# Kernel optimization log

Measured on AMD Instinct MI355X. Metric: run time of the kernel, lower is better.

The kernel has to match this reference:

```python
import jax, jax.numpy as jnp
import numpy as np
from jax import lax

WINDOW_SIZE = 11
EPS = 1e-6  # params.epsilon (external global in original repo)
FACTOR = 255.0  # 2**8 - 1
C1 = 0.01
C2 = 10.0
# Constants from TMQI paper (computed with numpy, static)
_CSF = 100.0 * 2.6 * (0.0192 + 0.114 * 16) * np.exp(-(0.114 * 16) ** 1.1)
U_HDR = 128.0 / (1.4 * _CSF)
SIG_HDR = U_HDR / 3.0
U_LDR = U_HDR
SIG_LDR = U_LDR / 3.0


def _norm_cdf(x, loc, scale):
    return 0.5 * (1.0 + lax.erf((x - loc) / (scale * np.sqrt(2.0).astype(np.float32))))


def _box_conv(x, w):
    # x: [B,1,H,W], w: [1,1,ws,ws] (uniform window summing to 1), VALID padding
    return lax.conv_general_dilated(
        x, w, window_strides=(1, 1), padding='VALID',
        dimension_numbers=('NCHW', 'OIHW', 'NCHW'))


def setup_inputs() -> dict:
    key = jax.random.key(0)
    k1, k2 = jax.random.split(key)
    img1 = jax.random.uniform(k1, (16, 1, 1024, 1024), dtype=jnp.float32)
    img2 = jax.random.uniform(k2, (16, 1, 1024, 1024), dtype=jnp.float32)
    return {"img1": img1, "img2": img2}


def reference(img1, img2):
    # create_window returns ones((1, channel, ws, ws)); normalized -> uniform 1/ws^2
    ws = WINDOW_SIZE
    window = jnp.ones((1, 1, ws, ws), dtype=img1.dtype) / (ws * ws)

    # Global min/max normalization to [0, 255]
    x1 = FACTOR * (img1 - img1.min()) / (img1.max() - img1.min() + EPS)
    x2 = FACTOR * (img2 - img2.min()) / (img2.max() - img2.min() + EPS)

    mu1 = _box_conv(x1, window)
    mu2 = _box_conv(x2, window)
    mu1_sq = mu1 * mu1
    mu2_sq = mu2 * mu2
    mu1_mu2 = mu1 * mu2

    sigma1_sq = _box_conv(x1 * x1, window) - mu1_sq
    sigma2_sq = _box_conv(x2 * x2, window) - mu2_sq
    sigma12 = _box_conv(x1 * x2, window) - mu1_mu2

    sigma1 = jnp.sqrt(jnp.maximum(sigma1_sq, 0.0) + EPS)
    sigma2 = jnp.sqrt(jnp.maximum(sigma2_sq, 0.0) + EPS)

    sigma1p = _norm_cdf(sigma1, U_HDR, SIG_HDR)
    sigma2p = _norm_cdf(sigma2, U_LDR, SIG_LDR)

    s_map = ((2.0 * sigma1p * sigma2p + C1) / (sigma1p ** 2 + sigma2p ** 2 + C1)
             * ((sigma12 + C2) / (sigma1 * sigma2 + C2)))
    # size_average=True -> scalar mean
    return s_map.mean()
```

## Files before the change

kernel.cpp:

```cpp
#include <hip/hip_runtime.h>
#include <math.h>

#define BATCH 16
#define H 1024
#define W 1024
#define WSZ 11
#define OH (H - WSZ + 1)
#define OW (W - WSZ + 1)
#define NPIX ((size_t)BATCH * H * W)

#define MM_BLOCKS 2048
#define MM_TPB 256
#define MM_PT 8

#define TPB 256
#define CPT 4
#define RSTRIP 8
#define NSTRIP ((OH + RSTRIP - 1) / RSTRIP)
#define TGRID (NSTRIP * BATCH)

#define WS_DPART(ws)  ((double*)(ws))
#define WS_MMPART(ws) ((float4*)((char*)(ws) + 16384))
#define WS_COEF(ws)   ((float*)((char*)(ws) + 49152))

__device__ __forceinline__ float min4(float4 v) {
  return fminf(fminf(v.x, v.y), fminf(v.z, v.w));
}
__device__ __forceinline__ float max4(float4 v) {
  return fmaxf(fmaxf(v.x, v.y), fmaxf(v.z, v.w));
}

__global__ void __launch_bounds__(MM_TPB) minmax_kernel(
    const float4* __restrict__ a4, const float4* __restrict__ b4,
    float4* __restrict__ part) {
  const int tid = threadIdx.x;
  const size_t base = (size_t)blockIdx.x * (MM_TPB * MM_PT) + tid;
  float4 A0 = a4[base], A1 = a4[base + 256], A2 = a4[base + 512], A3 = a4[base + 768];
  float4 A4 = a4[base + 1024], A5 = a4[base + 1280], A6 = a4[base + 1536], A7 = a4[base + 1792];
  float4 B0 = b4[base], B1 = b4[base + 256], B2 = b4[base + 512], B3 = b4[base + 768];
  float4 B4 = b4[base + 1024], B5 = b4[base + 1280], B6 = b4[base + 1536], B7 = b4[base + 1792];
  float mn1 = fminf(fminf(fminf(min4(A0), min4(A1)), fminf(min4(A2), min4(A3))),
                    fminf(fminf(min4(A4), min4(A5)), fminf(min4(A6), min4(A7))));
  float mx1 = fmaxf(fmaxf(fmaxf(max4(A0), max4(A1)), fmaxf(max4(A2), max4(A3))),
                    fmaxf(fmaxf(max4(A4), max4(A5)), fmaxf(max4(A6), max4(A7))));
  float mn2 = fminf(fminf(fminf(min4(B0), min4(B1)), fminf(min4(B2), min4(B3))),
                    fminf(fminf(min4(B4), min4(B5)), fminf(min4(B6), min4(B7))));
  float mx2 = fmaxf(fmaxf(fmaxf(max4(B0), max4(B1)), fmaxf(max4(B2), max4(B3))),
                    fmaxf(fmaxf(max4(B4), max4(B5)), fmaxf(max4(B6), max4(B7))));
#pragma unroll
  for (int off = 32; off > 0; off >>= 1) {
    mn1 = fminf(mn1, __shfl_down(mn1, off));
    mx1 = fmaxf(mx1, __shfl_down(mx1, off));
    mn2 = fminf(mn2, __shfl_down(mn2, off));
    mx2 = fmaxf(mx2, __shfl_down(mx2, off));
  }
  __shared__ float s[4][4];
  const int wave = tid >> 6, lane = tid & 63;
  if (lane == 0) { s[0][wave] = mn1; s[1][wave] = mx1; s[2][wave] = mn2; s[3][wave] = mx2; }
  __syncthreads();
  if (tid == 0) {
    mn1 = fminf(fminf(s[0][0], s[0][1]), fminf(s[0][2], s[0][3]));
    mx1 = fmaxf(fmaxf(s[1][0], s[1][1]), fmaxf(s[1][2], s[1][3]));
    mn2 = fminf(fminf(s[2][0], s[2][1]), fminf(s[2][2], s[2][3]));
    mx2 = fmaxf(fmaxf(s[3][0], s[3][1]), fmaxf(s[3][2], s[3][3]));
    part[blockIdx.x] = make_float4(mn1, mx1, mn2, mx2);
  }
}

__global__ void __launch_bounds__(256) reduce_minmax_kernel(
    const float4* __restrict__ part, float* __restrict__ coef) {
  const int tid = threadIdx.x;
  float mn1 = 1e30f, mx1 = -1e30f, mn2 = 1e30f, mx2 = -1e30f;
#pragma unroll
  for (int k = 0; k < MM_BLOCKS / 256; ++k) {
    float4 p = part[tid + k * 256];
    mn1 = fminf(mn1, p.x); mx1 = fmaxf(mx1, p.y);
    mn2 = fminf(mn2, p.z); mx2 = fmaxf(mx2, p.w);
  }
#pragma unroll
  for (int off = 32; off > 0; off >>= 1) {
    mn1 = fminf(mn1, __shfl_down(mn1, off));
    mx1 = fmaxf(mx1, __shfl_down(mx1, off));
    mn2 = fminf(mn2, __shfl_down(mn2, off));
    mx2 = fmaxf(mx2, __shfl_down(mx2, off));
  }
  __shared__ float s[4][4];
  const int wave = tid >> 6, lane = tid & 63;
  if (lane == 0) { s[0][wave] = mn1; s[1][wave] = mx1; s[2][wave] = mn2; s[3][wave] = mx2; }
  __syncthreads();
  if (tid == 0) {
    mn1 = fminf(fminf(s[0][0], s[0][1]), fminf(s[0][2], s[0][3]));
    mx1 = fmaxf(fmaxf(s[1][0], s[1][1]), fmaxf(s[1][2], s[1][3]));
    mn2 = fminf(fminf(s[2][0], s[2][1]), fminf(s[2][2], s[2][3]));
    mx2 = fmaxf(fmaxf(s[3][0], s[3][1]), fmaxf(s[3][2], s[3][3]));
    const float inv121 = 1.0f / 121.0f;
    float a1 = 255.0f / (mx1 - mn1 + 1e-6f);
    float a2 = 255.0f / (mx2 - mn2 + 1e-6f);
    coef[0] = a1 * a1 * inv121;
    coef[1] = a1 * a1 * inv121 * inv121;
    coef[2] = a2 * a2 * inv121;
    coef[3] = a2 * a2 * inv121 * inv121;
    coef[4] = a1 * a2 * inv121;
    coef[5] = a1 * a2 * inv121 * inv121;
  }
}

__global__ void __launch_bounds__(TPB, 4) tmqi_kernel(
    const float* __restrict__ img1, const float* __restrict__ img2,
    const float* __restrict__ coef, double* __restrict__ dpart,
    float uhdr, float inv_s, float Tsq) {
  __shared__ float cs[5][W];

  const int tid = threadIdx.x;
  const int r0 = blockIdx.x * RSTRIP;
  const int b = blockIdx.y;
  const int rs = min(RSTRIP, OH - r0);
  const int c = tid * CPT;

  const float cA2 = coef[0], cA1 = coef[1];
  const float cB2 = coef[2], cB1 = coef[3];
  const float cC2 = coef[4], cC1 = coef[5];

  const float* p1 = img1 + ((size_t)b << 20) + c;
  const float* p2 = img2 + ((size_t)b << 20) + c;

  float su[4], sv[4], suu[4], svv[4], suv[4];
#pragma unroll
  for (int k = 0; k < 4; ++k) { su[k] = sv[k] = suu[k] = svv[k] = suv[k] = 0.0f; }

#pragma unroll
  for (int j = 0; j < WSZ; ++j) {
    const int r = r0 + j;
    float4 u4 = *(const float4*)(p1 + ((size_t)r << 10));
    float4 v4 = *(const float4*)(p2 + ((size_t)r << 10));
    float uu[4] = {u4.x, u4.y, u4.z, u4.w};
    float vv[4] = {v4.x, v4.y, v4.z, v4.w};
#pragma unroll
    for (int k = 0; k < 4; ++k) {
      su[k] += uu[k]; sv[k] += vv[k];
      suu[k] = fmaf(uu[k], uu[k], suu[k]);
      svv[k] = fmaf(vv[k], vv[k], svv[k]);
      suv[k] = fmaf(uu[k], vv[k], suv[k]);
    }
  }

  double acc = 0.0;
  float4 un4, vn4, uo4, vo4;

#pragma unroll 1
  for (int i = 0; i < rs; ++i) {
    if (i > 0) {
      float un[4] = {un4.x, un4.y, un4.z, un4.w};
      float vn[4] = {vn4.x, vn4.y, vn4.z, vn4.w};
      float uo[4] = {uo4.x, uo4.y, uo4.z, uo4.w};
      float vo[4] = {vo4.x, vo4.y, vo4.z, vo4.w};
#pragma unroll
      for (int k = 0; k < 4; ++k) {
        su[k] += un[k] - uo[k];
        sv[k] += vn[k] - vo[k];
        suu[k] += fmaf(un[k], un[k], -uo[k] * uo[k]);
        svv[k] += fmaf(vn[k], vn[k], -vo[k] * vo[k]);
        suv[k] += fmaf(un[k], vn[k], -uo[k] * vo[k]);
      }
    }
    ((float4*)(cs[0]))[tid] = make_float4(su[0], su[1], su[2], su[3]);
    ((float4*)(cs[1]))[tid] = make_float4(sv[0], sv[1], sv[2], sv[3]);
    ((float4*)(cs[2]))[tid] = make_float4(suu[0], suu[1], suu[2], suu[3]);
    ((float4*)(cs[3]))[tid] = make_float4(svv[0], svv[1], svv[2], svv[3]);
    ((float4*)(cs[4]))[tid] = make_float4(suv[0], suv[1], suv[2], suv[3]);
    __syncthreads();

    if (i + 1 < rs) {
      const int rn = r0 + i + WSZ;
      const int ro = r0 + i;
      un4 = *(const float4*)(p1 + ((size_t)rn << 10));
      vn4 = *(const float4*)(p2 + ((size_t)rn << 10));
      uo4 = *(const float4*)(p1 + ((size_t)ro << 10));
      vo4 = *(const float4*)(p2 + ((size_t)ro << 10));
    }

    if (c < OW) {
      const bool w3ok = (c + 12 < W);
      float S[5][4];
#pragma unroll
      for (int q = 0; q < 5; ++q) {
        const float* row = cs[q];
        float4 w0 = *(const float4*)(row + c);
        float4 w1 = *(const float4*)(row + c + 4);
        float4 w2 = *(const float4*)(row + c + 8);
        float4 w3 = w3ok ? *(const float4*)(row + c + 12) : make_float4(0.f, 0.f, 0.f, 0.f);
        float s0 = w0.x + w0.y + w0.z + w0.w + w1.x + w1.y + w1.z + w1.w +
                   w2.x + w2.y + w2.z;
        S[q][0] = s0;
        float s1 = s0 - w0.x + w2.w; S[q][1] = s1;
        float s2 = s1 - w0.y + w3.x; S[q][2] = s2;
        float s3 = s2 - w0.z + w3.y; S[q][3] = s3;
      }
      float rowacc = 0.0f;
#pragma unroll
      for (int k = 0; k < 4; ++k) {
        if (c + k < OW) {
          float m1 = cA1 * S[0][k];
          float s1sq = fmaf(-m1, S[0][k], cA2 * S[2][k]);
          float m2 = cB1 * S[1][k];
          float s2sq = fmaf(-m2, S[1][k], cB2 * S[3][k]);
          float m3 = cC1 * S[0][k];
          float s12  = fmaf(-m3, S[1][k], cC2 * S[4][k]);
          float A  = fmaxf(s1sq, 0.0f) + 1e-6f;
          float Bq = fmaxf(s2sq, 0.0f) + 1e-6f;
          float sgp = __builtin_amdgcn_sqrtf(A * Bq);
          float smap = (s12 + 10.0f) * __builtin_amdgcn_rcpf(sgp + 10.0f);
          if (__builtin_expect(!(A >= Tsq && Bq >= Tsq), 0)) {
            float sg1 = sqrtf(A), sg2 = sqrtf(Bq);
            float pp1 = 0.5f * (1.0f + erff((sg1 - uhdr) * inv_s));
            float pp2 = 0.5f * (1.0f + erff((sg2 - uhdr) * inv_s));
            float ratio1 = (2.0f * pp1 * pp2 + 0.01f) / (pp1 * pp1 + pp2 * pp2 + 0.01f);
            smap = ratio1 * ((s12 + 10.0f) / (sg1 * sg2 + 10.0f));
          }
          rowacc += smap;
        }
      }
      acc += (double)rowacc;
    }
    __syncthreads();
  }

#pragma unroll
  for (int off = 32; off > 0; off >>= 1) acc += __shfl_down(acc, off);
  double* wred = (double*)cs;
  __syncthreads();
  if ((tid & 63) == 0) wred[tid >> 6] = acc;
  __syncthreads();
  if (tid == 0) {
    dpart[blockIdx.y * NSTRIP + blockIdx.x] = wred[0] + wred[1] + wred[2] + wred[3];
  }
}

__global__ void __launch_bounds__(256) finalize_kernel(
    const double* __restrict__ dpart, float* __restrict__ out) {
  const int tid = threadIdx.x;
  double acc = 0.0;
  for (int i = tid; i < TGRID; i += 256) acc += dpart[i];
#pragma unroll
  for (int off = 32; off > 0; off >>= 1) acc += __shfl_down(acc, off);
  __shared__ double s[4];
  const int wave = tid >> 6, lane = tid & 63;
  if (lane == 0) s[wave] = acc;
  __syncthreads();
  if (tid == 0) {
    double total = s[0] + s[1] + s[2] + s[3];
    out[0] = (float)(total / (double)((size_t)BATCH * OH * OW));
  }
}

extern "C" void kernel_launch(void* const* d_in, const int* in_sizes, int n_in,
                              void* d_out, int out_size, void* d_ws, size_t ws_size,
                              hipStream_t stream) {
  const float* img1 = (const float*)d_in[0];
  const float* img2 = (const float*)d_in[1];
  float* out = (float*)d_out;

  double* dpart = WS_DPART(d_ws);
  float4* mmpart = WS_MMPART(d_ws);
  float* coef = WS_COEF(d_ws);

  const double csf = 100.0 * 2.6 * (0.0192 + 0.114 * 16.0) * exp(-pow(0.114 * 16.0, 1.1));
  const double u_hdr = 128.0 / (1.4 * csf);
  const double sig_hdr = u_hdr / 3.0;
  const float uhdr = (float)u_hdr;
  const float inv_s = (float)(1.0 / (sig_hdr * sqrt(2.0)));
  const double T = u_hdr + 4.0 * sig_hdr * sqrt(2.0);
  const float Tsq = (float)(T * T);

  hipLaunchKernelGGL(minmax_kernel, dim3(MM_BLOCKS), dim3(MM_TPB), 0, stream,
                     (const float4*)img1, (const float4*)img2, mmpart);
  hipLaunchKernelGGL(reduce_minmax_kernel, dim3(1), dim3(256), 0, stream, mmpart, coef);
  dim3 grid(NSTRIP, BATCH);
  hipLaunchKernelGGL(tmqi_kernel, grid, dim3(TPB), 0, stream,
                     img1, img2, coef, dpart, uhdr, inv_s, Tsq);
  hipLaunchKernelGGL(finalize_kernel, dim3(1), dim3(256), 0, stream, dpart, out);
}
```

Before: 211.5 us.

## Double-buffer column sums in LDS, drop trailing barrier, read own sums from registers

Column-sum rows are now double-buffered in shared memory, so only one barrier per output row is needed instead of two. Each thread takes its own four column sums from registers and reads only the neighbours' values from LDS, which cuts LDS traffic. The strip height changes to 13 so that 1014 rows divide evenly, which removes the tail handling. The cost is twice the LDS footprint, which may limit occupancy.

```diff
diff --git a/kernel.cpp b/kernel.cpp
--- a/kernel.cpp
+++ b/kernel.cpp
@@ -15,8 +15,8 @@
 
 #define TPB 256
 #define CPT 4
-#define RSTRIP 8
-#define NSTRIP ((OH + RSTRIP - 1) / RSTRIP)
+#define RSTRIP 13
+#define NSTRIP (OH / RSTRIP)
 #define TGRID (NSTRIP * BATCH)
 
 #define WS_DPART(ws)  ((double*)(ws))
@@ -109,12 +109,12 @@
     const float* __restrict__ img1, const float* __restrict__ img2,
     const float* __restrict__ coef, double* __restrict__ dpart,
     float uhdr, float inv_s, float Tsq) {
-  __shared__ float cs[5][W];
+  __shared__ float cs[2][5][W];
 
   const int tid = threadIdx.x;
   const int r0 = blockIdx.x * RSTRIP;
   const int b = blockIdx.y;
-  const int rs = min(RSTRIP, OH - r0);
+  const int rs = RSTRIP;
   const int c = tid * CPT;
 
   const float cA2 = coef[0], cA1 = coef[1];
@@ -149,6 +149,7 @@
 
 #pragma unroll 1
   for (int i = 0; i < rs; ++i) {
+    const int p = i & 1;
     if (i > 0) {
       float un[4] = {un4.x, un4.y, un4.z, un4.w};
       float vn[4] = {vn4.x, vn4.y, vn4.z, vn4.w};
@@ -163,11 +164,11 @@
         suv[k] += fmaf(un[k], vn[k], -uo[k] * vo[k]);
       }
     }
-    ((float4*)(cs[0]))[tid] = make_float4(su[0], su[1], su[2], su[3]);
-    ((float4*)(cs[1]))[tid] = make_float4(sv[0], sv[1], sv[2], sv[3]);
-    ((float4*)(cs[2]))[tid] = make_float4(suu[0], suu[1], suu[2], suu[3]);
-    ((float4*)(cs[3]))[tid] = make_float4(svv[0], svv[1], svv[2], svv[3]);
-    ((float4*)(cs[4]))[tid] = make_float4(suv[0], suv[1], suv[2], suv[3]);
+    ((float4*)(cs[p][0]))[tid] = make_float4(su[0], su[1], su[2], su[3]);
+    ((float4*)(cs[p][1]))[tid] = make_float4(sv[0], sv[1], sv[2], sv[3]);
+    ((float4*)(cs[p][2]))[tid] = make_float4(suu[0], suu[1], suu[2], suu[3]);
+    ((float4*)(cs[p][3]))[tid] = make_float4(svv[0], svv[1], svv[2], svv[3]);
+    ((float4*)(cs[p][4]))[tid] = make_float4(suv[0], suv[1], suv[2], suv[3]);
     __syncthreads();
 
     if (i + 1 < rs) {
@@ -180,32 +181,42 @@
     }
 
     if (c < OW) {
-      const bool w3ok = (c + 12 < W);
-      float S[5][4];
+      const bool w3ok = (tid <= 252);
+      float W0a[5], W1a[5], W2a[5], W3a[5];
+      float own[5][4] = {{su[0], su[1], su[2], su[3]},
+                         {sv[0], sv[1], sv[2], sv[3]},
+                         {suu[0], suu[1], suu[2], suu[3]},
+                         {svv[0], svv[1], svv[2], svv[3]},
+                         {suv[0], suv[1], suv[2], suv[3]}};
 #pragma unroll
       for (int q = 0; q < 5; ++q) {
-        const float* row = cs[q];
-        float4 w0 = *(const float4*)(row + c);
-        float4 w1 = *(const float4*)(row + c + 4);
-        float4 w2 = *(const float4*)(row + c + 8);
-        float4 w3 = w3ok ? *(const float4*)(row + c + 12) : make_float4(0.f, 0.f, 0.f, 0.f);
-        float s0 = w0.x + w0.y + w0.z + w0.w + w1.x + w1.y + w1.z + w1.w +
-                   w2.x + w2.y + w2.z;
-        S[q][0] = s0;
-        float s1 = s0 - w0.x + w2.w; S[q][1] = s1;
-        float s2 = s1 - w0.y + w3.x; S[q][2] = s2;
-        float s3 = s2 - w0.z + w3.y; S[q][3] = s3;
+        const float* row = cs[p][q];
+        float4 w1 = ((const float4*)row)[tid + 1];
+        float4 w2 = ((const float4*)row)[tid + 2];
+        float2 w3 = w3ok ? ((const float2*)row)[2 * (tid + 3)]
+                         : make_float2(0.f, 0.f);
+        float s0 = own[q][0] + own[q][1] + own[q][2] + own[q][3] +
+                   w1.x + w1.y + w1.z + w1.w + w2.x + w2.y + w2.z;
+        W0a[q] = s0;
+        float s1 = s0 - own[q][0] + w2.w; W1a[q] = s1;
+        float s2 = s1 - own[q][1] + w3.x; W2a[q] = s2;
+        float s3 = s2 - own[q][2] + w3.y; W3a[q] = s3;
       }
       float rowacc = 0.0f;
 #pragma unroll
       for (int k = 0; k < 4; ++k) {
+        float S0 = (k == 0) ? W0a[0] : (k == 1) ? W1a[0] : (k == 2) ? W2a[0] : W3a[0];
+        float S1 = (k == 0) ? W0a[1] : (k == 1) ? W1a[1] : (k == 2) ? W2a[1] : W3a[1];
+        float S2 = (k == 0) ? W0a[2] : (k == 1) ? W1a[2] : (k == 2) ? W2a[2] : W3a[2];
+        float S3 = (k == 0) ? W0a[3] : (k == 1) ? W1a[3] : (k == 2) ? W2a[3] : W3a[3];
+        float S4 = (k == 0) ? W0a[4] : (k == 1) ? W1a[4] : (k == 2) ? W2a[4] : W3a[4];
         if (c + k < OW) {
-          float m1 = cA1 * S[0][k];
-          float s1sq = fmaf(-m1, S[0][k], cA2 * S[2][k]);
-          float m2 = cB1 * S[1][k];
-          float s2sq = fmaf(-m2, S[1][k], cB2 * S[3][k]);
-          float m3 = cC1 * S[0][k];
-          float s12  = fmaf(-m3, S[1][k], cC2 * S[4][k]);
+          float m1 = cA1 * S0;
+          float s1sq = fmaf(-m1, S0, cA2 * S2);
+          float m2 = cB1 * S1;
+          float s2sq = fmaf(-m2, S1, cB2 * S3);
+          float m3 = cC1 * S0;
+          float s12  = fmaf(-m3, S1, cC2 * S4);
           float A  = fmaxf(s1sq, 0.0f) + 1e-6f;
           float Bq = fmaxf(s2sq, 0.0f) + 1e-6f;
           float sgp = __builtin_amdgcn_sqrtf(A * Bq);
@@ -222,7 +233,6 @@
       }
       acc += (double)rowacc;
     }
-    __syncthreads();
   }
 
 #pragma unroll
```

Result: faster. 201.1 us (-4.9%).

## Make each wave own a full row strip with register-resident horizontal sliding sums

Applied to the files above, without the earlier changes.

Each wavefront now handles a 13-row strip across the full image width, with 16 columns per lane. Column sums stay in registers and the horizontal window sum slides along the lane's columns, using a cross-lane shuffle for the halo. This removes the shared-memory staging and both __syncthreads per output row, and per-wave results are written directly without a block reduction. The cost is much higher register pressure (80 accumulators plus double-buffered loads), which may cut occupancy, and the changed strip size makes 1014/13 divide exactly.

```diff
diff --git a/kernel.cpp b/kernel.cpp
--- a/kernel.cpp
+++ b/kernel.cpp
@@ -7,17 +7,16 @@
 #define WSZ 11
 #define OH (H - WSZ + 1)
 #define OW (W - WSZ + 1)
-#define NPIX ((size_t)BATCH * H * W)
 
 #define MM_BLOCKS 2048
 #define MM_TPB 256
 #define MM_PT 8
 
 #define TPB 256
-#define CPT 4
-#define RSTRIP 8
-#define NSTRIP ((OH + RSTRIP - 1) / RSTRIP)
-#define TGRID (NSTRIP * BATCH)
+#define RSTRIP 13
+#define NSTRIP (OH / RSTRIP)
+#define NWAVES (NSTRIP * BATCH)
+#define TBLOCKS (NWAVES / 4)
 
 #define WS_DPART(ws)  ((double*)(ws))
 #define WS_MMPART(ws) ((float4*)((char*)(ws) + 16384))
@@ -105,142 +104,155 @@
   }
 }
 
-__global__ void __launch_bounds__(TPB, 4) tmqi_kernel(
+#define LOADROW(DU, DV, r) do {                                             \
+    const float* _ru = p1 + ((size_t)(r) << 10);                            \
+    const float* _rv = p2 + ((size_t)(r) << 10);                            \
+    DU[0] = *(const float4*)(_ru + 0);  DU[1] = *(const float4*)(_ru + 4);  \
+    DU[2] = *(const float4*)(_ru + 8);  DU[3] = *(const float4*)(_ru + 12); \
+    DV[0] = *(const float4*)(_rv + 0);  DV[1] = *(const float4*)(_rv + 4);  \
+    DV[2] = *(const float4*)(_rv + 8);  DV[3] = *(const float4*)(_rv + 12); \
+  } while (0)
+
+__device__ __forceinline__ void integ4(float S[5][16], int base, float4 u, float4 v) {
+  float uu[4] = {u.x, u.y, u.z, u.w};
+  float vv[4] = {v.x, v.y, v.z, v.w};
+#pragma unroll
+  for (int e = 0; e < 4; ++e) {
+    float a = uu[e], bb = vv[e];
+    S[0][base + e] += a;
+    S[1][base + e] += bb;
+    S[2][base + e] = fmaf(a, a, S[2][base + e]);
+    S[3][base + e] = fmaf(bb, bb, S[3][base + e]);
+    S[4][base + e] = fmaf(a, bb, S[4][base + e]);
+  }
+}
+
+__device__ __forceinline__ void slide4(float S[5][16], int base,
+                                       float4 un, float4 vn, float4 uo, float4 vo) {
+  float a[4] = {un.x, un.y, un.z, un.w};
+  float b[4] = {vn.x, vn.y, vn.z, vn.w};
+  float c[4] = {uo.x, uo.y, uo.z, uo.w};
+  float d[4] = {vo.x, vo.y, vo.z, vo.w};
+#pragma unroll
+  for (int e = 0; e < 4; ++e) {
+    S[0][base + e] += a[e] - c[e];
+    S[1][base + e] += b[e] - d[e];
+    S[2][base + e] += fmaf(a[e], a[e], -c[e] * c[e]);
+    S[3][base + e] += fmaf(b[e], b[e], -d[e] * d[e]);
+    S[4][base + e] += fmaf(a[e], b[e], -c[e] * d[e]);
+  }
+}
+
+__device__ __forceinline__ float mapfun(const float Wq[5],
+                                        float cA2, float cA1, float cB2, float cB1,
+                                        float cC2, float cC1,
+                                        float uhdr, float inv_s, float Tsq) {
+  float m1 = cA1 * Wq[0];
+  float s1sq = fmaf(-m1, Wq[0], cA2 * Wq[2]);
+  float m2 = cB1 * Wq[1];
+  float s2sq = fmaf(-m2, Wq[1], cB2 * Wq[3]);
+  float m3 = cC1 * Wq[0];
+  float s12  = fmaf(-m3, Wq[1], cC2 * Wq[4]);
+  float A  = fmaxf(s1sq, 0.0f) + 1e-6f;
+  float Bq = fmaxf(s2sq, 0.0f) + 1e-6f;
+  float sgp = __builtin_amdgcn_sqrtf(A * Bq);
+  float smap = (s12 + 10.0f) * __builtin_amdgcn_rcpf(sgp + 10.0f);
+  if (__builtin_expect(!(A >= Tsq && Bq >= Tsq), 0)) {
+    float sg1 = sqrtf(A), sg2 = sqrtf(Bq);
+    float pp1 = 0.5f * (1.0f + erff((sg1 - uhdr) * inv_s));
+    float pp2 = 0.5f * (1.0f + erff((sg2 - uhdr) * inv_s));
+    float ratio1 = (2.0f * pp1 * pp2 + 0.01f) / (pp1 * pp1 + pp2 * pp2 + 0.01f);
+    smap = ratio1 * ((s12 + 10.0f) / (sg1 * sg2 + 10.0f));
+  }
+  return smap;
+}
+
+__global__ void __launch_bounds__(TPB) tmqi_kernel(
     const float* __restrict__ img1, const float* __restrict__ img2,
     const float* __restrict__ coef, double* __restrict__ dpart,
     float uhdr, float inv_s, float Tsq) {
-  __shared__ float cs[5][W];
-
-  const int tid = threadIdx.x;
-  const int r0 = blockIdx.x * RSTRIP;
-  const int b = blockIdx.y;
-  const int rs = min(RSTRIP, OH - r0);
-  const int c = tid * CPT;
+  const int tid = threadIdx.x;
+  const int lane = tid & 63;
+  const int wid = blockIdx.x * 4 + (tid >> 6);
+  const int b = wid / NSTRIP;
+  const int s = wid - b * NSTRIP;
+  const int r0 = s * RSTRIP;
+  const int c0 = lane * 16;
 
   const float cA2 = coef[0], cA1 = coef[1];
   const float cB2 = coef[2], cB1 = coef[3];
   const float cC2 = coef[4], cC1 = coef[5];
 
-  const float* p1 = img1 + ((size_t)b << 20) + c;
-  const float* p2 = img2 + ((size_t)b << 20) + c;
-
-  float su[4], sv[4], suu[4], svv[4], suv[4];
-#pragma unroll
-  for (int k = 0; k < 4; ++k) { su[k] = sv[k] = suu[k] = svv[k] = suv[k] = 0.0f; }
-
-#pragma unroll
-  for (int j = 0; j < WSZ; ++j) {
-    const int r = r0 + j;
-    float4 u4 = *(const float4*)(p1 + ((size_t)r << 10));
-    float4 v4 = *(const float4*)(p2 + ((size_t)r << 10));
-    float uu[4] = {u4.x, u4.y, u4.z, u4.w};
-    float vv[4] = {v4.x, v4.y, v4.z, v4.w};
-#pragma unroll
-    for (int k = 0; k < 4; ++k) {
-      su[k] += uu[k]; sv[k] += vv[k];
-      suu[k] = fmaf(uu[k], uu[k], suu[k]);
-      svv[k] = fmaf(vv[k], vv[k], svv[k]);
-      suv[k] = fmaf(uu[k], vv[k], suv[k]);
+  const float* p1 = img1 + ((size_t)b << 20) + c0;
+  const float* p2 = img2 + ((size_t)b << 20) + c0;
+
+  float S[5][16];
+#pragma unroll
+  for (int j = 0; j < 16; ++j) {
+    S[0][j] = S[1][j] = S[2][j] = S[3][j] = S[4][j] = 0.0f;
+  }
+
+  {
+    float4 CU[2][4], CV[2][4];
+    LOADROW(CU[0], CV[0], r0);
+#pragma unroll
+    for (int j = 0; j < WSZ; ++j) {
+      const int p = j & 1;
+      if (j + 1 < WSZ) LOADROW(CU[p ^ 1], CV[p ^ 1], r0 + j + 1);
+#pragma unroll
+      for (int c4 = 0; c4 < 4; ++c4) integ4(S, c4 * 4, CU[p][c4], CV[p][c4]);
     }
   }
 
   double acc = 0.0;
-  float4 un4, vn4, uo4, vo4;
 
 #pragma unroll 1
-  for (int i = 0; i < rs; ++i) {
-    if (i > 0) {
-      float un[4] = {un4.x, un4.y, un4.z, un4.w};
-      float vn[4] = {vn4.x, vn4.y, vn4.z, vn4.w};
-      float uo[4] = {uo4.x, uo4.y, uo4.z, uo4.w};
-      float vo[4] = {vo4.x, vo4.y, vo4.z, vo4.w};
-#pragma unroll
-      for (int k = 0; k < 4; ++k) {
-        su[k] += un[k] - uo[k];
-        sv[k] += vn[k] - vo[k];
-        suu[k] += fmaf(un[k], un[k], -uo[k] * uo[k]);
-        svv[k] += fmaf(vn[k], vn[k], -vo[k] * vo[k]);
-        suv[k] += fmaf(un[k], vn[k], -uo[k] * vo[k]);
+  for (int i = 0; i < RSTRIP; ++i) {
+    float4 NU[4], NV[4], OU[4], OV[4];
+    const bool more = (i + 1 < RSTRIP);
+    if (more) {
+      LOADROW(NU, NV, r0 + i + WSZ);
+      LOADROW(OU, OV, r0 + i);
+    }
+
+    float Wq[5];
+#pragma unroll
+    for (int q = 0; q < 5; ++q) {
+      float t = S[q][0];
+#pragma unroll
+      for (int j = 1; j <= 10; ++j) t += S[q][j];
+      Wq[q] = t;
+    }
+    float rowacc = mapfun(Wq, cA2, cA1, cB2, cB1, cC2, cC1, uhdr, inv_s, Tsq);
+#pragma unroll
+    for (int k = 1; k < 16; ++k) {
+#pragma unroll
+      for (int q = 0; q < 5; ++q) {
+        float add = (k + 10 < 16) ? S[q][k + 10] : __shfl_down(S[q][k - 6], 1);
+        Wq[q] += add - S[q][k - 1];
       }
-    }
-    ((float4*)(cs[0]))[tid] = make_float4(su[0], su[1], su[2], su[3]);
-    ((float4*)(cs[1]))[tid] = make_float4(sv[0], sv[1], sv[2], sv[3]);
-    ((float4*)(cs[2]))[tid] = make_float4(suu[0], suu[1], suu[2], suu[3]);
-    ((float4*)(cs[3]))[tid] = make_float4(svv[0], svv[1], svv[2], svv[3]);
-    ((float4*)(cs[4]))[tid] = make_float4(suv[0], suv[1], suv[2], suv[3]);
-    __syncthreads();
-
-    if (i + 1 < rs) {
-      const int rn = r0 + i + WSZ;
-      const int ro = r0 + i;
-      un4 = *(const float4*)(p1 + ((size_t)rn << 10));
-      vn4 = *(const float4*)(p2 + ((size_t)rn << 10));
-      uo4 = *(const float4*)(p1 + ((size_t)ro << 10));
-      vo4 = *(const float4*)(p2 + ((size_t)ro << 10));
-    }
-
-    if (c < OW) {
-      const bool w3ok = (c + 12 < W);
-      float S[5][4];
-#pragma unroll
-      for (int q = 0; q < 5; ++q) {
-        const float* row = cs[q];
-        float4 w0 = *(const float4*)(row + c);
-        float4 w1 = *(const float4*)(row + c + 4);
-        float4 w2 = *(const float4*)(row + c + 8);
-        float4 w3 = w3ok ? *(const float4*)(row + c + 12) : make_float4(0.f, 0.f, 0.f, 0.f);
-        float s0 = w0.x + w0.y + w0.z + w0.w + w1.x + w1.y + w1.z + w1.w +
-                   w2.x + w2.y + w2.z;
-        S[q][0] = s0;
-        float s1 = s0 - w0.x + w2.w; S[q][1] = s1;
-        float s2 = s1 - w0.y + w3.x; S[q][2] = s2;
-        float s3 = s2 - w0.z + w3.y; S[q][3] = s3;
-      }
-      float rowacc = 0.0f;
-#pragma unroll
-      for (int k = 0; k < 4; ++k) {
-        if (c + k < OW) {
-          float m1 = cA1 * S[0][k];
-          float s1sq = fmaf(-m1, S[0][k], cA2 * S[2][k]);
-          float m2 = cB1 * S[1][k];
-          float s2sq = fmaf(-m2, S[1][k], cB2 * S[3][k]);
-          float m3 = cC1 * S[0][k];
-          float s12  = fmaf(-m3, S[1][k], cC2 * S[4][k]);
-          float A  = fmaxf(s1sq, 0.0f) + 1e-6f;
-          float Bq = fmaxf(s2sq, 0.0f) + 1e-6f;
-          float sgp = __builtin_amdgcn_sqrtf(A * Bq);
-          float smap = (s12 + 10.0f) * __builtin_amdgcn_rcpf(sgp + 10.0f);
-          if (__builtin_expect(!(A >= Tsq && Bq >= Tsq), 0)) {
-            float sg1 = sqrtf(A), sg2 = sqrtf(Bq);
-            float pp1 = 0.5f * (1.0f + erff((sg1 - uhdr) * inv_s));
-            float pp2 = 0.5f * (1.0f + erff((sg2 - uhdr) * inv_s));
-            float ratio1 = (2.0f * pp1 * pp2 + 0.01f) / (pp1 * pp1 + pp2 * pp2 + 0.01f);
-            smap = ratio1 * ((s12 + 10.0f) / (sg1 * sg2 + 10.0f));
-          }
-          rowacc += smap;
-        }
-      }
-      acc += (double)rowacc;
-    }
-    __syncthreads();
+      float sm = mapfun(Wq, cA2, cA1, cB2, cB1, cC2, cC1, uhdr, inv_s, Tsq);
+      rowacc += (c0 + k < OW) ? sm : 0.0f;
+    }
+    acc += (double)rowacc;
+
+    if (more) {
+#pragma unroll
+      for (int c4 = 0; c4 < 4; ++c4)
+        slide4(S, c4 * 4, NU[c4], NV[c4], OU[c4], OV[c4]);
+    }
   }
 
 #pragma unroll
   for (int off = 32; off > 0; off >>= 1) acc += __shfl_down(acc, off);
-  double* wred = (double*)cs;
-  __syncthreads();
-  if ((tid & 63) == 0) wred[tid >> 6] = acc;
-  __syncthreads();
-  if (tid == 0) {
-    dpart[blockIdx.y * NSTRIP + blockIdx.x] = wred[0] + wred[1] + wred[2] + wred[3];
-  }
+  if (lane == 0) dpart[wid] = acc;
 }
 
 __global__ void __launch_bounds__(256) finalize_kernel(
     const double* __restrict__ dpart, float* __restrict__ out) {
   const int tid = threadIdx.x;
   double acc = 0.0;
-  for (int i = tid; i < TGRID; i += 256) acc += dpart[i];
+  for (int i = tid; i < NWAVES; i += 256) acc += dpart[i];
 #pragma unroll
   for (int off = 32; off > 0; off >>= 1) acc += __shfl_down(acc, off);
   __shared__ double s[4];
@@ -275,8 +287,7 @@
   hipLaunchKernelGGL(minmax_kernel, dim3(MM_BLOCKS), dim3(MM_TPB), 0, stream,
                      (const float4*)img1, (const float4*)img2, mmpart);
   hipLaunchKernelGGL(reduce_minmax_kernel, dim3(1), dim3(256), 0, stream, mmpart, coef);
-  dim3 grid(NSTRIP, BATCH);
-  hipLaunchKernelGGL(tmqi_kernel, grid, dim3(TPB), 0, stream,
+  hipLaunchKernelGGL(tmqi_kernel, dim3(TBLOCKS), dim3(TPB), 0, stream,
                      img1, img2, coef, dpart, uhdr, inv_s, Tsq);
   hipLaunchKernelGGL(finalize_kernel, dim3(1), dim3(256), 0, stream, dpart, out);
 }
```

After: 251.4 us. 18.9% more time.
